# Kernel optimization log

Measured on AMD Instinct MI355X. Metric: run time of the kernel, lower is better.

Reference implementation:

```python
import jax, jax.numpy as jnp
import numpy as np

NX = 2048
NL = 20
BATCH = 512
EIGMAX = 10.0
EPS = 1e-9


def prox_cardan(eta, x):
    """Prox of u -> -eta*(log(u)+log(1-u)) at x: unique root in (0,1) of
    u^3 - (1+x)u^2 + (x-2eta)u + eta = 0 (Cardano / trigonometric method)."""
    b = -(1.0 + x)
    c = x - 2.0 * eta
    d = eta
    p = c - b * b / 3.0
    q = 2.0 * b ** 3 / 27.0 - b * c / 3.0 + d
    disc = -4.0 * p ** 3 - 27.0 * q ** 2
    # three-real-roots branch (trigonometric); requires p<0
    pm = jnp.minimum(p, -1e-12)
    m = 2.0 * jnp.sqrt(-pm / 3.0)
    arg = jnp.clip(3.0 * q / (pm * m), -1.0, 1.0)
    th = jnp.arccos(arg)
    k = jnp.arange(3, dtype=x.dtype)
    t_trig = m[..., None] * jnp.cos((th[..., None] - 2.0 * jnp.pi * k) / 3.0)
    r_trig = t_trig - b[..., None] / 3.0
    in01 = (r_trig > 0.0) & (r_trig < 1.0)
    idx = jnp.argmax(in01, axis=-1)
    root3 = jnp.take_along_axis(r_trig, idx[..., None], axis=-1)[..., 0]
    # one-real-root branch
    s = jnp.sqrt(jnp.maximum(q * q / 4.0 + p ** 3 / 27.0, 0.0))
    root1 = jnp.cbrt(-q / 2.0 + s) + jnp.cbrt(-q / 2.0 - s) - b / 3.0
    u = jnp.where(disc >= 0.0, root3, root1)
    return jnp.clip(u, EPS, 1.0 - EPS)


def setup_inputs() -> dict:
    key = jax.random.key(0)
    k1, k2, k3, k4, k5 = jax.random.split(key, 5)
    x = jax.random.uniform(k1, (BATCH, 1, NX), dtype=jnp.float32)
    # symmetric PSD operators for T^T T and D^T D (as in a discretized inverse problem)
    A = jax.random.normal(k2, (NX, NX), dtype=jnp.float32)
    tTT = (A @ A.T) / NX
    B = jax.random.normal(k3, (NX, NX), dtype=jnp.float32)
    tDD = (B @ B.T) / NX
    # orthogonal change-of-basis: element <-> eigen bases
    Q, _ = jnp.linalg.qr(jax.random.normal(k4, (NX, NX), dtype=jnp.float32))
    Pelt = Q.astype(jnp.float32)
    Peig = Q.T.astype(jnp.float32)
    x_b = jnp.einsum('ij,bcj->bci', tTT, x) + 0.01 * jax.random.normal(k5, (BATCH, 1, NX), dtype=jnp.float32)
    gamma = jnp.full((NL,), 0.1, dtype=jnp.float32)   # nn.Parameter([0.1])
    mu = jnp.zeros((NL,), dtype=jnp.float32)          # nn.Parameter([0.0])
    reg = jnp.full((NL,), 0.001, dtype=jnp.float32)   # noisy=True -> trainable 0.001
    return {"x": x, "x_b": x_b, "tDD": tDD, "tTT": tTT, "Peig": Peig,
            "Pelt": Pelt, "gamma": gamma, "mu": mu, "reg": reg}


def reference(x, x_b, tDD, tTT, Peig, Pelt, gamma, mu, reg):
    def step(xc, params):
        g_raw, mu_raw, reg_raw = params
        g = jax.nn.softplus(g_raw)
        mu_l = jax.nn.softplus(mu_raw) / 1e6
        reg_l = jax.nn.softplus(reg_raw) / (EIGMAX ** 2)
        grad = (jnp.einsum('ij,bcj->bci', tTT, xc) - x_b
                + reg_l * jnp.einsum('ij,bcj->bci', tDD, xc))
        xt = xc - g * grad
        xt = jnp.einsum('ij,bcj->bci', Pelt, xt)
        xt = prox_cardan(g * mu_l, xt)
        xt = jnp.einsum('ij,bcj->bci', Peig, xt)
        return xt, None

    out, _ = jax.lax.scan(step, x, (gamma, mu, reg))
    return out
```

## Files before the change

### kernel.cpp

```cpp
#include <hip/hip_runtime.h>
#include <math.h>

#define MDIM 512
#define NDIM 2048
#define KDIM 2048
#define NLAYERS 20

static const size_t MN = (size_t)MDIM * NDIM;
static const size_t OPN = (size_t)KDIM * KDIM;

using bf16x8 = __attribute__((ext_vector_type(8))) short;
using f32x4  = __attribute__((ext_vector_type(4))) float;

__device__ __forceinline__ double softplusd(double v) {
    return (v > 20.0) ? v : log1p(exp(v));
}

__device__ __forceinline__ float prox_cardan_f(float eta, float x) {
    const float b  = -(1.0f + x);
    const float c  = x - 2.0f * eta;
    const float dd = eta;
    const float p  = c - b * b * (1.0f / 3.0f);
    const float q  = 2.0f * b * b * b * (1.0f / 27.0f) - b * c * (1.0f / 3.0f) + dd;
    const float disc = -4.0f * p * p * p - 27.0f * q * q;
    const float pm = fminf(p, -1e-12f);
    const float mm = 2.0f * sqrtf(-pm * (1.0f / 3.0f));
    float arg = 3.0f * q / (pm * mm);
    arg = fminf(fmaxf(arg, -1.0f), 1.0f);
    const float th = acosf(arg);
    const float TWO_PI = 6.28318530717958647692f;
    const float r0 = mm * cosf(th * (1.0f / 3.0f)) - b * (1.0f / 3.0f);
    const float r1 = mm * cosf((th - TWO_PI) * (1.0f / 3.0f)) - b * (1.0f / 3.0f);
    const float r2 = mm * cosf((th - 2.0f * TWO_PI) * (1.0f / 3.0f)) - b * (1.0f / 3.0f);
    const bool in0 = (r0 > 0.0f) && (r0 < 1.0f);
    const bool in1 = (r1 > 0.0f) && (r1 < 1.0f);
    const bool in2 = (r2 > 0.0f) && (r2 < 1.0f);
    const float root3 = in0 ? r0 : (in1 ? r1 : (in2 ? r2 : r0));
    const float s = sqrtf(fmaxf(q * q * 0.25f + p * p * p * (1.0f / 27.0f), 0.0f));
    const float root1 = cbrtf(-q * 0.5f + s) + cbrtf(-q * 0.5f - s) - b * (1.0f / 3.0f);
    const float u = (disc >= 0.0f) ? root3 : root1;
    return fminf(fmaxf(u, 1e-9f), 1.0f - 1e-9f);
}

__device__ __forceinline__ double prox_newton_d(double eta, double x) {
    double u = (double)prox_cardan_f((float)eta, (float)x);
#pragma unroll
    for (int i = 0; i < 4; ++i) {
        const double um1 = u - 1.0;
        const double umx = u - x;
        const double P  = u * um1 * umx - eta * (2.0 * u - 1.0);
        const double dP = um1 * umx + u * umx + u * um1 - 2.0 * eta;
        u = u - P / dP;
        u = fmin(fmax(u, 1e-12), 1.0 - 1e-12);
    }
    return fmin(fmax(u, 1e-9), 1.0 - 1e-9);
}

__device__ __forceinline__ unsigned short f2bf(float f) {
    unsigned u = __float_as_uint(f);
    unsigned r = (u + 0x7FFFu + ((u >> 16) & 1u)) >> 16;
    return (unsigned short)r;
}
__device__ __forceinline__ float bf2f(unsigned short h) {
    return __uint_as_float(((unsigned)h) << 16);
}
__device__ __forceinline__ void split3f(float f, unsigned short& b1,
                                        unsigned short& b2, unsigned short& b3) {
    b1 = f2bf(f);
    const float r1 = f - bf2f(b1);
    b2 = f2bf(r1);
    const float r2 = r1 - bf2f(b2);
    b3 = f2bf(r2);
}

__device__ __forceinline__ void gl16(const void* g, void* l) {
    __builtin_amdgcn_global_load_lds(
        (const __attribute__((address_space(1))) unsigned int*)g,
        (__attribute__((address_space(3))) unsigned int*)l, 16, 0, 0);
}

__global__ __launch_bounds__(256) void split3_op(
    const float* __restrict__ s1, const float* __restrict__ s2,
    const float* __restrict__ greg, int layer,
    unsigned short* __restrict__ p1, unsigned short* __restrict__ p2,
    unsigned short* __restrict__ p3) {
    const size_t i = ((size_t)blockIdx.x * 256 + threadIdx.x) * 4;
    float reglf = 0.0f;
    if (s2) reglf = (float)(softplusd((double)greg[layer]) * 0.01);
    const float4 a = *(const float4*)(s1 + i);
    float4 b = make_float4(0.f, 0.f, 0.f, 0.f);
    if (s2) b = *(const float4*)(s2 + i);
    ushort4 o1, o2, o3;
    split3f(fmaf(reglf, b.x, a.x), o1.x, o2.x, o3.x);
    split3f(fmaf(reglf, b.y, a.y), o1.y, o2.y, o3.y);
    split3f(fmaf(reglf, b.z, a.z), o1.z, o2.z, o3.z);
    split3f(fmaf(reglf, b.w, a.w), o1.w, o2.w, o3.w);
    *(ushort4*)(p1 + i) = o1;
    *(ushort4*)(p2 + i) = o2;
    *(ushort4*)(p3 + i) = o3;
}

__global__ __launch_bounds__(256) void split3_w(
    const float* __restrict__ s1, const float* __restrict__ s2,
    const float* __restrict__ greg, int layer,
    unsigned short* __restrict__ p1, unsigned short* __restrict__ p2,
    unsigned short* __restrict__ p3) {
    if (layer > 0 && greg[layer] == greg[0]) return;
    const size_t i = ((size_t)blockIdx.x * 256 + threadIdx.x) * 4;
    const float reglf = (float)(softplusd((double)greg[layer]) * 0.01);
    const float4 a = *(const float4*)(s1 + i);
    const float4 b = *(const float4*)(s2 + i);
    ushort4 o1, o2, o3;
    split3f(fmaf(reglf, b.x, a.x), o1.x, o2.x, o3.x);
    split3f(fmaf(reglf, b.y, a.y), o1.y, o2.y, o3.y);
    split3f(fmaf(reglf, b.z, a.z), o1.z, o2.z, o3.z);
    split3f(fmaf(reglf, b.w, a.w), o1.w, o2.w, o3.w);
    *(ushort4*)(p1 + i) = o1;
    *(ushort4*)(p2 + i) = o2;
    *(ushort4*)(p3 + i) = o3;
}

__global__ __launch_bounds__(256, 3) void gemm_bf16x3(
    const unsigned short* __restrict__ A1, const unsigned short* __restrict__ A2,
    const unsigned short* __restrict__ A3,
    const unsigned short* __restrict__ W1, const unsigned short* __restrict__ W2,
    const unsigned short* __restrict__ W3,
    float* __restrict__ Part, int klen, int S) {
    __shared__ __align__(16) unsigned short Ab[2][3][64][32];
    __shared__ __align__(16) unsigned short Wb[2][3][64][32];

    const int tid = threadIdx.x;

    const int nwg = 256 * S;
    const int cpx = nwg >> 3;
    const int bid = blockIdx.x;
    const int g   = (bid & 7) * cpx + (bid >> 3);
    const int xs  = g / (8 * S);
    const int rr  = g - xs * (8 * S);
    const int ys  = rr & 7;
    const int zs  = rr >> 3;
    const int n0 = xs * 64;
    const int m0 = ys * 64;
    const int kb = zs * klen;

    const int lane = tid & 63, wid = tid >> 6;
    const int quad = lane >> 4, lrow = lane & 15;
    const int wm = (wid >> 1) * 32, wn = (wid & 1) * 32;

    const int srow = tid >> 2;
    const int lc8  = ((tid & 3) ^ ((tid >> 3) & 3)) * 8;
    const int t8   = tid * 8;
    const int qx   = (quad ^ ((lrow >> 1) & 3)) * 8;

    const unsigned short* gA1 = A1 + (size_t)(m0 + srow) * KDIM + kb + lc8;
    const unsigned short* gA2 = A2 + (size_t)(m0 + srow) * KDIM + kb + lc8;
    const unsigned short* gA3 = A3 + (size_t)(m0 + srow) * KDIM + kb + lc8;
    const unsigned short* gW1 = W1 + (size_t)(n0 + srow) * KDIM + kb + lc8;
    const unsigned short* gW2 = W2 + (size_t)(n0 + srow) * KDIM + kb + lc8;
    const unsigned short* gW3 = W3 + (size_t)(n0 + srow) * KDIM + kb + lc8;

    unsigned short* lA = &Ab[0][0][0][0];
    unsigned short* lW = &Wb[0][0][0][0];

    f32x4 ahi[2][2], alo[2][2];
#pragma unroll
    for (int a = 0; a < 2; ++a)
#pragma unroll
        for (int b = 0; b < 2; ++b) {
            ahi[a][b] = (f32x4){0.f, 0.f, 0.f, 0.f};
            alo[a][b] = (f32x4){0.f, 0.f, 0.f, 0.f};
        }

    gl16(gA1, lA + t8);
    gl16(gA2, lA + 2048 + t8);
    gl16(gA3, lA + 4096 + t8);
    gl16(gW1, lW + t8);
    gl16(gW2, lW + 2048 + t8);
    gl16(gW3, lW + 4096 + t8);

    int cur = 0;
    for (int k0 = 0; k0 < klen; k0 += 32) {
        __syncthreads();

        if (k0 + 32 < klen) {
            const int nb = (cur ^ 1) * 6144;
            gl16(gA1 + k0 + 32, lA + nb + t8);
            gl16(gA2 + k0 + 32, lA + nb + 2048 + t8);
            gl16(gA3 + k0 + 32, lA + nb + 4096 + t8);
            gl16(gW1 + k0 + 32, lW + nb + t8);
            gl16(gW2 + k0 + 32, lW + nb + 2048 + t8);
            gl16(gW3 + k0 + 32, lW + nb + 4096 + t8);
        }

        const unsigned short* cA = lA + cur * 6144;
        const unsigned short* cW = lW + cur * 6144;

        bf16x8 fa[2][3], fw[2][3];
#pragma unroll
        for (int t = 0; t < 2; ++t) {
            const int ra = (wm + t * 16 + lrow) * 32;
            const int rw = (wn + t * 16 + lrow) * 32;
            fa[t][0] = *(const bf16x8*)(cA + ra + qx);
            fa[t][1] = *(const bf16x8*)(cA + 2048 + ra + qx);
            fa[t][2] = *(const bf16x8*)(cA + 4096 + ra + qx);
            fw[t][0] = *(const bf16x8*)(cW + rw + qx);
            fw[t][1] = *(const bf16x8*)(cW + 2048 + rw + qx);
            fw[t][2] = *(const bf16x8*)(cW + 4096 + rw + qx);
        }
#pragma unroll
        for (int tm = 0; tm < 2; ++tm)
#pragma unroll
            for (int tn = 0; tn < 2; ++tn) {
                ahi[tm][tn] = __builtin_amdgcn_mfma_f32_16x16x32_bf16(fa[tm][0], fw[tn][0], ahi[tm][tn], 0, 0, 0);
                alo[tm][tn] = __builtin_amdgcn_mfma_f32_16x16x32_bf16(fa[tm][0], fw[tn][1], alo[tm][tn], 0, 0, 0);
                alo[tm][tn] = __builtin_amdgcn_mfma_f32_16x16x32_bf16(fa[tm][1], fw[tn][0], alo[tm][tn], 0, 0, 0);
                alo[tm][tn] = __builtin_amdgcn_mfma_f32_16x16x32_bf16(fa[tm][1], fw[tn][1], alo[tm][tn], 0, 0, 0);
                alo[tm][tn] = __builtin_amdgcn_mfma_f32_16x16x32_bf16(fa[tm][0], fw[tn][2], alo[tm][tn], 0, 0, 0);
                alo[tm][tn] = __builtin_amdgcn_mfma_f32_16x16x32_bf16(fa[tm][2], fw[tn][0], alo[tm][tn], 0, 0, 0);
            }
        cur ^= 1;
    }

    float* P = Part + (size_t)zs * MN;
#pragma unroll
    for (int tm = 0; tm < 2; ++tm)
#pragma unroll
        for (int tn = 0; tn < 2; ++tn) {
            const int mbase = m0 + wm + tm * 16 + quad * 4;
            const int nn = n0 + wn + tn * 16 + lrow;
#pragma unroll
            for (int r = 0; r < 4; ++r)
                P[(size_t)(mbase + r) * NDIM + nn] = ahi[tm][tn][r] + alo[tm][tn][r];
        }
}

template <int MODE>
__global__ __launch_bounds__(256) void combine3(
    const float* __restrict__ Part, int S,
    const float* __restrict__ Xc, const float* __restrict__ Xb,
    float* __restrict__ stateOut,
    unsigned short* __restrict__ p1, unsigned short* __restrict__ p2,
    unsigned short* __restrict__ p3,
    const float* __restrict__ gam, const float* __restrict__ gmu,
    const float* __restrict__ greg, int layer) {
    const size_t i = ((size_t)blockIdx.x * 256 + threadIdx.x) * 4;
    double s0 = 0.0, s1 = 0.0, s2 = 0.0, s3 = 0.0;
    for (int z = 0; z < S; ++z) {
        const float4 p = *(const float4*)(Part + (size_t)z * MN + i);
        s0 += (double)p.x; s1 += (double)p.y; s2 += (double)p.z; s3 += (double)p.w;
    }
    float v0, v1, v2, v3;
    if (MODE == 0) {
        const double g = softplusd((double)gam[layer]);
        const float4 xc = *(const float4*)(Xc + i);
        const float4 xb = *(const float4*)(Xb + i);
        v0 = (float)((double)xc.x - g * (s0 - (double)xb.x));
        v1 = (float)((double)xc.y - g * (s1 - (double)xb.y));
        v2 = (float)((double)xc.z - g * (s2 - (double)xb.z));
        v3 = (float)((double)xc.w - g * (s3 - (double)xb.w));
    } else if (MODE == 1) {
        const double g   = softplusd((double)gam[layer]);
        const double eta = g * softplusd((double)gmu[layer]) * 1e-6;
        v0 = (float)prox_newton_d(eta, s0);
        v1 = (float)prox_newton_d(eta, s1);
        v2 = (float)prox_newton_d(eta, s2);
        v3 = (float)prox_newton_d(eta, s3);
    } else {
        v0 = (float)s0; v1 = (float)s1; v2 = (float)s2; v3 = (float)s3;
        *(float4*)(stateOut + i) = make_float4(v0, v1, v2, v3);
    }
    ushort4 o1, o2, o3;
    split3f(v0, o1.x, o2.x, o3.x);
    split3f(v1, o1.y, o2.y, o3.y);
    split3f(v2, o1.z, o2.z, o3.z);
    split3f(v3, o1.w, o2.w, o3.w);
    *(ushort4*)(p1 + i) = o1;
    *(ushort4*)(p2 + i) = o2;
    *(ushort4*)(p3 + i) = o3;
}

#define BM 64
#define BN 64
#define BK 32
#define LDSP 68

__device__ __forceinline__ double prox_cardan_d(double eta, double x) {
    const double b  = -(1.0 + x);
    const double c  = x - 2.0 * eta;
    const double dd = eta;
    const double p  = c - b * b * (1.0 / 3.0);
    const double q  = 2.0 * b * b * b * (1.0 / 27.0) - b * c * (1.0 / 3.0) + dd;
    const double disc = -4.0 * p * p * p - 27.0 * q * q;
    const double pm = fmin(p, -1e-12);
    const double mm = 2.0 * sqrt(-pm * (1.0 / 3.0));
    double arg = 3.0 * q / (pm * mm);
    arg = fmin(fmax(arg, -1.0), 1.0);
    const double th = acos(arg);
    const double TWO_PI = 6.283185307179586476925286766559;
    const double r0 = mm * cos(th * (1.0 / 3.0)) - b * (1.0 / 3.0);
    const double r1 = mm * cos((th - TWO_PI) * (1.0 / 3.0)) - b * (1.0 / 3.0);
    const double r2 = mm * cos((th - 2.0 * TWO_PI) * (1.0 / 3.0)) - b * (1.0 / 3.0);
    const bool in0 = (r0 > 0.0) && (r0 < 1.0);
    const bool in1 = (r1 > 0.0) && (r1 < 1.0);
    const bool in2 = (r2 > 0.0) && (r2 < 1.0);
    const double root3 = in0 ? r0 : (in1 ? r1 : (in2 ? r2 : r0));
    const double s = sqrt(fmax(q * q * 0.25 + p * p * p * (1.0 / 27.0), 0.0));
    const double root1 = cbrt(-q * 0.5 + s) + cbrt(-q * 0.5 - s) - b * (1.0 / 3.0);
    const double u = (disc >= 0.0) ? root3 : root1;
    return fmin(fmax(u, 1e-9), 1.0 - 1e-9);
}

template <bool FUSE2>
__global__ __launch_bounds__(256, 4) void gemm_nt_splitk(
    const float* __restrict__ A, const float* __restrict__ W1,
    const float* __restrict__ W2, double* __restrict__ Part,
    const float* __restrict__ greg, int layer, int klen) {
    __shared__ float As[BK][LDSP];
    __shared__ float Ws[BK][LDSP];
    const int tid = threadIdx.x;
    const int m0 = blockIdx.y * BM;
    const int n0 = blockIdx.x * BN;
    const int kbase = blockIdx.z * klen;
    float reglf = 0.0f;
    if (FUSE2) reglf = (float)(softplusd((double)greg[layer]) * 0.01);
    const int lrow = tid >> 3;
    const int lkc  = (tid & 7) << 2;
    const float* pA  = A  + (size_t)(m0 + lrow) * KDIM + kbase + lkc;
    const float* pW  = W1 + (size_t)(n0 + lrow) * KDIM + kbase + lkc;
    const float* pW2 = FUSE2 ? (W2 + (size_t)(n0 + lrow) * KDIM + kbase + lkc) : nullptr;
    float4 ra[2], rw[2];
    ra[0] = *(const float4*)(pA);
    ra[1] = *(const float4*)(pA + 32 * KDIM);
    rw[0] = *(const float4*)(pW);
    rw[1] = *(const float4*)(pW + 32 * KDIM);
    if (FUSE2) {
        const float4 u0 = *(const float4*)(pW2);
        const float4 u1 = *(const float4*)(pW2 + 32 * KDIM);
        rw[0].x += reglf * u0.x; rw[0].y += reglf * u0.y;
        rw[0].z += reglf * u0.z; rw[0].w += reglf * u0.w;
        rw[1].x += reglf * u1.x; rw[1].y += reglf * u1.y;
        rw[1].z += reglf * u1.z; rw[1].w += reglf * u1.w;
    }
    float  acc[4][4]   = {};
    double acc64[4][4] = {};
    const int tx = (tid & 15) << 2;
    const int ty = (tid >> 4) << 2;
    int it = 0;
    for (int k0 = 0; k0 < klen; k0 += BK, ++it) {
#pragma unroll
        for (int h = 0; h < 2; ++h) {
            const int row = lrow + (h << 5);
            As[lkc + 0][row] = (h ? ra[1].x : ra[0].x);
            As[lkc + 1][row] = (h ? ra[1].y : ra[0].y);
            As[lkc + 2][row] = (h ? ra[1].z : ra[0].z);
            As[lkc + 3][row] = (h ? ra[1].w : ra[0].w);
            Ws[lkc + 0][row] = (h ? rw[1].x : rw[0].x);
            Ws[lkc + 1][row] = (h ? rw[1].y : rw[0].y);
            Ws[lkc + 2][row] = (h ? rw[1].z : rw[0].z);
            Ws[lkc + 3][row] = (h ? rw[1].w : rw[0].w);
        }
        __syncthreads();
        if (k0 + BK < klen) {
            const float* qA = pA + k0 + BK;
            ra[0] = *(const float4*)(qA);
            ra[1] = *(const float4*)(qA + 32 * KDIM);
            const float* qW = pW + k0 + BK;
            rw[0] = *(const float4*)(qW);
            rw[1] = *(const float4*)(qW + 32 * KDIM);
            if (FUSE2) {
                const float* qW2 = pW2 + k0 + BK;
                const float4 u0 = *(const float4*)(qW2);
                const float4 u1 = *(const float4*)(qW2 + 32 * KDIM);
                rw[0].x += reglf * u0.x; rw[0].y += reglf * u0.y;
                rw[0].z += reglf * u0.z; rw[0].w += reglf * u0.w;
                rw[1].x += reglf * u1.x; rw[1].y += reglf * u1.y;
                rw[1].z += reglf * u1.z; rw[1].w += reglf * u1.w;
            }
        }
#pragma unroll
        for (int kk = 0; kk < BK; ++kk) {
            const float4 a4 = *(const float4*)(&As[kk][ty]);
            const float4 b4 = *(const float4*)(&Ws[kk][tx]);
            const float av[4] = {a4.x, a4.y, a4.z, a4.w};
            const float bv[4] = {b4.x, b4.y, b4.z, b4.w};
#pragma unroll
            for (int r = 0; r < 4; ++r)
#pragma unroll
                for (int cc = 0; cc < 4; ++cc)
                    acc[r][cc] = fmaf(av[r], bv[cc], acc[r][cc]);
        }
        __syncthreads();
        if ((it & 1) == 1) {
#pragma unroll
            for (int r = 0; r < 4; ++r)
#pragma unroll
                for (int cc = 0; cc < 4; ++cc) {
                    acc64[r][cc] += (double)acc[r][cc];
                    acc[r][cc] = 0.0f;
                }
        }
    }
#pragma unroll
    for (int r = 0; r < 4; ++r)
#pragma unroll
        for (int cc = 0; cc < 4; ++cc)
            acc64[r][cc] += (double)acc[r][cc];
    double* Pz = Part + (size_t)blockIdx.z * MN;
#pragma unroll
    for (int r = 0; r < 4; ++r) {
        double* q = Pz + (size_t)(m0 + ty + r) * NDIM + n0 + tx;
        *(double2*)(q)     = make_double2(acc64[r][0], acc64[r][1]);
        *(double2*)(q + 2) = make_double2(acc64[r][2], acc64[r][3]);
    }
}

template <int MODE>
__global__ __launch_bounds__(256) void combine_ep(
    const double* __restrict__ Part, int nslices,
    const float* __restrict__ Xc, const float* __restrict__ Xb,
    float* __restrict__ Out,
    const float* __restrict__ gam, const float* __restrict__ gmu,
    const float* __restrict__ greg, int layer) {
    const size_t i4 = ((size_t)blockIdx.x * 256 + threadIdx.x) * 4;
    double s0 = 0.0, s1 = 0.0, s2 = 0.0, s3 = 0.0;
    for (int z = 0; z < nslices; ++z) {
        const double* p = Part + (size_t)z * MN + i4;
        const double2 a = *(const double2*)(p);
        const double2 b = *(const double2*)(p + 2);
        s0 += a.x; s1 += a.y; s2 += b.x; s3 += b.y;
    }
    float4 o;
    if (MODE == 0) {
        const double g = softplusd((double)gam[layer]);
        const float4 xc = *(const float4*)(Xc + i4);
        const float4 xb = *(const float4*)(Xb + i4);
        o.x = (float)((double)xc.x - g * (s0 - (double)xb.x));
        o.y = (float)((double)xc.y - g * (s1 - (double)xb.y));
        o.z = (float)((double)xc.z - g * (s2 - (double)xb.z));
        o.w = (float)((double)xc.w - g * (s3 - (double)xb.w));
    } else if (MODE == 1) {
        const double g   = softplusd((double)gam[layer]);
        const double eta = g * softplusd((double)gmu[layer]) * 1e-6;
        o.x = (float)prox_cardan_d(eta, s0);
        o.y = (float)prox_cardan_d(eta, s1);
        o.z = (float)prox_cardan_d(eta, s2);
        o.w = (float)prox_cardan_d(eta, s3);
    } else {
        o.x = (float)s0; o.y = (float)s1; o.z = (float)s2; o.w = (float)s3;
    }
    *(float4*)(Out + i4) = o;
}

extern "C" void kernel_launch(void* const* d_in, const int* in_sizes, int n_in,
                              void* d_out, int out_size, void* d_ws, size_t ws_size,
                              hipStream_t stream) {
    const float* x    = (const float*)d_in[0];
    const float* x_b  = (const float*)d_in[1];
    const float* tDD  = (const float*)d_in[2];
    const float* tTT  = (const float*)d_in[3];
    const float* Peig = (const float*)d_in[4];
    const float* Pelt = (const float*)d_in[5];
    const float* gam  = (const float*)d_in[6];
    const float* gmu  = (const float*)d_in[7];
    const float* greg = (const float*)d_in[8];
    float* out = (float*)d_out;

    const size_t TRI_OP_B = 3 * OPN * 2;
    const size_t TRI_A_B  = 3 * MN * 2;
    const size_t STATE_B  = MN * 4;
    const size_t full_need = 3 * TRI_OP_B + 2 * TRI_A_B + STATE_B + 2 * MN * 4;
    const size_t mid_need  = 1 * TRI_OP_B + 2 * TRI_A_B + STATE_B + 2 * MN * 4;

    const bool full = (ws_size >= full_need);
    const bool mid  = (!full && ws_size >= mid_need);

    if (full || mid) {
        const int S = 2;
        const int klen = KDIM / S;
        char* p = (char*)d_ws;
        unsigned short *Wt1, *Wt2, *Wt3, *Pe1, *Pe2, *Pe3, *Pg1, *Pg2, *Pg3;
        if (full) {
            Wt1 = (unsigned short*)p;        Wt2 = Wt1 + OPN; Wt3 = Wt2 + OPN; p += TRI_OP_B;
            Pe1 = (unsigned short*)p;        Pe2 = Pe1 + OPN; Pe3 = Pe2 + OPN; p += TRI_OP_B;
            Pg1 = (unsigned short*)p;        Pg2 = Pg1 + OPN; Pg3 = Pg2 + OPN; p += TRI_OP_B;
        } else {
            Wt1 = (unsigned short*)p;        Wt2 = Wt1 + OPN; Wt3 = Wt2 + OPN; p += TRI_OP_B;
            Pe1 = Wt1; Pe2 = Wt2; Pe3 = Wt3;
            Pg1 = Wt1; Pg2 = Wt2; Pg3 = Wt3;
        }
        unsigned short* Aa1 = (unsigned short*)p; unsigned short* Aa2 = Aa1 + MN;
        unsigned short* Aa3 = Aa2 + MN; p += TRI_A_B;
        unsigned short* Ab1 = (unsigned short*)p; unsigned short* Ab2 = Ab1 + MN;
        unsigned short* Ab3 = Ab2 + MN; p += TRI_A_B;
        float* state = (float*)p; p += STATE_B;
        float* part  = (float*)p;

        const dim3 gg((unsigned)(256 * S));
        const unsigned cgrid = (unsigned)(MN / 4 / 256);
        const unsigned ogrid = (unsigned)(OPN / 4 / 256);

        split3_op<<<cgrid, 256, 0, stream>>>(x, nullptr, greg, 0, Aa1, Aa2, Aa3);
        if (full) {
            split3_op<<<ogrid, 256, 0, stream>>>(Pelt, nullptr, greg, 0, Pe1, Pe2, Pe3);
            split3_op<<<ogrid, 256, 0, stream>>>(Peig, nullptr, greg, 0, Pg1, Pg2, Pg3);
        }

        unsigned short *c1 = Aa1, *c2 = Aa2, *c3 = Aa3;
        unsigned short *d1 = Ab1, *d2 = Ab2, *d3 = Ab3;

        for (int l = 0; l < NLAYERS; ++l) {
            if (full) {
                split3_w<<<ogrid, 256, 0, stream>>>(tTT, tDD, greg, l, Wt1, Wt2, Wt3);
            } else {
                split3_op<<<ogrid, 256, 0, stream>>>(tTT, tDD, greg, l, Wt1, Wt2, Wt3);
            }
            gemm_bf16x3<<<gg, 256, 0, stream>>>(c1, c2, c3, Wt1, Wt2, Wt3, part, klen, S);
            combine3<0><<<cgrid, 256, 0, stream>>>(part, S, (l == 0 ? x : state), x_b,
                                                   nullptr, d1, d2, d3, gam, gmu, greg, l);
            if (mid) split3_op<<<ogrid, 256, 0, stream>>>(Pelt, nullptr, greg, 0, Pe1, Pe2, Pe3);
            gemm_bf16x3<<<gg, 256, 0, stream>>>(d1, d2, d3, Pe1, Pe2, Pe3, part, klen, S);
            combine3<1><<<cgrid, 256, 0, stream>>>(part, S, nullptr, nullptr,
                                                   nullptr, c1, c2, c3, gam, gmu, greg, l);
            if (mid) split3_op<<<ogrid, 256, 0, stream>>>(Peig, nullptr, greg, 0, Pg1, Pg2, Pg3);
            gemm_bf16x3<<<gg, 256, 0, stream>>>(c1, c2, c3, Pg1, Pg2, Pg3, part, klen, S);
            combine3<2><<<cgrid, 256, 0, stream>>>(part, S, nullptr, nullptr,
                                                   (l == NLAYERS - 1 ? out : state),
                                                   d1, d2, d3, gam, gmu, greg, l);
            unsigned short* t;
            t = c1; c1 = d1; d1 = t;
            t = c2; c2 = d2; d2 = t;
            t = c3; c3 = d3; d3 = t;
        }
        return;
    }

    char* wsb = (char*)d_ws;
    float* b0 = (float*)wsb;
    float* b1 = b0 + MN;
    float* b2 = b1 + MN;
    float* b3 = b2 + MN;
    const size_t base_bytes = 4 * MN * sizeof(float);
    double* partd = (double*)(wsb + base_bytes);
    int S = 0;
    if (ws_size >= base_bytes + 2 * MN * sizeof(double)) S = 2;
    else if (ws_size >= base_bytes + 1 * MN * sizeof(double)) S = 1;
    if (S == 0) return;
    const int klen = KDIM / S;
    dim3 gg(NDIM / BN, MDIM / BM, S);
    dim3 cg((unsigned)(MN / 4 / 256));
    const float* cur = x;
    float* bx = b0; float* bu = b1; float* bn = b2; float* bo = b3;
    for (int l = 0; l < NLAYERS; ++l) {
        gemm_nt_splitk<true><<<gg, 256, 0, stream>>>(cur, tTT, tDD, partd, greg, l, klen);
        combine_ep<0><<<cg, 256, 0, stream>>>(partd, S, cur, x_b, bx, gam, gmu, greg, l);
        gemm_nt_splitk<false><<<gg, 256, 0, stream>>>(bx, Pelt, nullptr, partd, greg, l, klen);
        combine_ep<1><<<cg, 256, 0, stream>>>(partd, S, nullptr, nullptr, bu, gam, gmu, greg, l);
        gemm_nt_splitk<false><<<gg, 256, 0, stream>>>(bu, Peig, nullptr, partd, greg, l, klen);
        float* dst = (l == NLAYERS - 1) ? out : bn;
        combine_ep<2><<<cg, 256, 0, stream>>>(partd, S, nullptr, nullptr, dst, gam, gmu, greg, l);
        cur = bn;
        float* t = bn; bn = bo; bo = t;
    }
}
```

Measured before the change: 2.620 ms.

## Triple-buffer LDS in bf16x3 GEMM with explicit vmcnt waits and MFMA priority

Replaces the double-buffered K loop of the split-bf16 GEMM with a three-stage LDS ring, prefetching two steps ahead and using explicit s_waitcnt vmcnt counts plus a raw barrier instead of __syncthreads. MFMA sections are wrapped in s_setprio to favour compute issue. The extra stage raises LDS use per block, so launch bounds drop from 3 to 2 blocks per CU, trading occupancy for deeper latency hiding. The hand-written vmcnt(6) assumes exactly six outstanding loads per stage, which is fragile if gl16 lowers to a different number of memory ops.

```diff
diff --git a/kernel.cpp b/kernel.cpp
--- a/kernel.cpp
+++ b/kernel.cpp
@@ -120,14 +120,14 @@
     *(ushort4*)(p3 + i) = o3;
 }
 
-__global__ __launch_bounds__(256, 3) void gemm_bf16x3(
+__global__ __launch_bounds__(256, 2) void gemm_bf16x3(
     const unsigned short* __restrict__ A1, const unsigned short* __restrict__ A2,
     const unsigned short* __restrict__ A3,
     const unsigned short* __restrict__ W1, const unsigned short* __restrict__ W2,
     const unsigned short* __restrict__ W3,
     float* __restrict__ Part, int klen, int S) {
-    __shared__ __align__(16) unsigned short Ab[2][3][64][32];
-    __shared__ __align__(16) unsigned short Wb[2][3][64][32];
+    __shared__ __align__(16) unsigned short Ab[3][3][64][32];
+    __shared__ __align__(16) unsigned short Wb[3][3][64][32];
 
     const int tid = threadIdx.x;
 
@@ -171,29 +171,39 @@
             alo[a][b] = (f32x4){0.f, 0.f, 0.f, 0.f};
         }
 
-    gl16(gA1, lA + t8);
-    gl16(gA2, lA + 2048 + t8);
-    gl16(gA3, lA + 4096 + t8);
-    gl16(gW1, lW + t8);
-    gl16(gW2, lW + 2048 + t8);
-    gl16(gW3, lW + 4096 + t8);
-
-    int cur = 0;
-    for (int k0 = 0; k0 < klen; k0 += 32) {
-        __syncthreads();
-
-        if (k0 + 32 < klen) {
-            const int nb = (cur ^ 1) * 6144;
-            gl16(gA1 + k0 + 32, lA + nb + t8);
-            gl16(gA2 + k0 + 32, lA + nb + 2048 + t8);
-            gl16(gA3 + k0 + 32, lA + nb + 4096 + t8);
-            gl16(gW1 + k0 + 32, lW + nb + t8);
-            gl16(gW2 + k0 + 32, lW + nb + 2048 + t8);
-            gl16(gW3 + k0 + 32, lW + nb + 4096 + t8);
-        }
-
-        const unsigned short* cA = lA + cur * 6144;
-        const unsigned short* cW = lW + cur * 6144;
+    auto stage = [&](int buf, int step) {
+        const int off = buf * 6144;
+        const int ko  = step * 32;
+        gl16(gA1 + ko, lA + off + t8);
+        gl16(gA2 + ko, lA + off + 2048 + t8);
+        gl16(gA3 + ko, lA + off + 4096 + t8);
+        gl16(gW1 + ko, lW + off + t8);
+        gl16(gW2 + ko, lW + off + 2048 + t8);
+        gl16(gW3 + ko, lW + off + 4096 + t8);
+    };
+
+    const int nsteps = klen >> 5;
+
+    stage(0, 0);
+    if (nsteps > 1) stage(1, 1);
+
+    int idx = 0;
+    for (int s = 0; s < nsteps; ++s) {
+        if (s + 1 < nsteps) {
+            asm volatile("s_waitcnt vmcnt(6)" ::: "memory");
+        } else {
+            asm volatile("s_waitcnt vmcnt(0)" ::: "memory");
+        }
+        __builtin_amdgcn_s_barrier();
+        __builtin_amdgcn_sched_barrier(0);
+
+        if (s + 2 < nsteps) {
+            int pre = idx + 2; if (pre >= 3) pre -= 3;
+            stage(pre, s + 2);
+        }
+
+        const unsigned short* cA = lA + idx * 6144;
+        const unsigned short* cW = lW + idx * 6144;
 
         bf16x8 fa[2][3], fw[2][3];
 #pragma unroll
@@ -207,6 +217,7 @@
             fw[t][1] = *(const bf16x8*)(cW + 2048 + rw + qx);
             fw[t][2] = *(const bf16x8*)(cW + 4096 + rw + qx);
         }
+        __builtin_amdgcn_s_setprio(1);
 #pragma unroll
         for (int tm = 0; tm < 2; ++tm)
 #pragma unroll
@@ -218,7 +229,9 @@
                 alo[tm][tn] = __builtin_amdgcn_mfma_f32_16x16x32_bf16(fa[tm][0], fw[tn][2], alo[tm][tn], 0, 0, 0);
                 alo[tm][tn] = __builtin_amdgcn_mfma_f32_16x16x32_bf16(fa[tm][2], fw[tn][0], alo[tm][tn], 0, 0, 0);
             }
-        cur ^= 1;
+        __builtin_amdgcn_s_setprio(0);
+
+        ++idx; if (idx == 3) idx = 0;
     }
 
     float* P = Part + (size_t)zs * MN;
```

Result: slower. 2.719 ms (+3.8%).

## Replace async LDS DMA double-buffer with register-staged prefetch and 64-wide K tiles

Applied to the files above, without the earlier changes.

The GEMM main loop no longer uses global_load_lds double buffering with 32-wide K slices. It now prefetches the next 64-wide K tile into registers while computing on a single XOR-swizzled LDS buffer, and raises MFMA priority with s_setprio. Occupancy hint drops from 3 to 2 blocks per CU. The goal is fewer barriers per K step and better overlap of global loads with MFMA, at the cost of more registers and a serial store-then-compute phase per tile.

```diff
diff --git a/kernel.cpp b/kernel.cpp
--- a/kernel.cpp
+++ b/kernel.cpp
@@ -73,12 +73,6 @@
     b3 = f2bf(r2);
 }
 
-__device__ __forceinline__ void gl16(const void* g, void* l) {
-    __builtin_amdgcn_global_load_lds(
-        (const __attribute__((address_space(1))) unsigned int*)g,
-        (__attribute__((address_space(3))) unsigned int*)l, 16, 0, 0);
-}
-
 __global__ __launch_bounds__(256) void split3_op(
     const float* __restrict__ s1, const float* __restrict__ s2,
     const float* __restrict__ greg, int layer,
@@ -120,14 +114,14 @@
     *(ushort4*)(p3 + i) = o3;
 }
 
-__global__ __launch_bounds__(256, 3) void gemm_bf16x3(
+__global__ __launch_bounds__(256, 2) void gemm_bf16x3(
     const unsigned short* __restrict__ A1, const unsigned short* __restrict__ A2,
     const unsigned short* __restrict__ A3,
     const unsigned short* __restrict__ W1, const unsigned short* __restrict__ W2,
     const unsigned short* __restrict__ W3,
     float* __restrict__ Part, int klen, int S) {
-    __shared__ __align__(16) unsigned short Ab[2][3][64][32];
-    __shared__ __align__(16) unsigned short Wb[2][3][64][32];
+    __shared__ __align__(16) unsigned short Ab[3][64][64];
+    __shared__ __align__(16) unsigned short Wb[3][64][64];
 
     const int tid = threadIdx.x;
 
@@ -148,77 +142,95 @@
     const int wm = (wid >> 1) * 32, wn = (wid & 1) * 32;
 
     const int srow = tid >> 2;
-    const int lc8  = ((tid & 3) ^ ((tid >> 3) & 3)) * 8;
-    const int t8   = tid * 8;
-    const int qx   = (quad ^ ((lrow >> 1) & 3)) * 8;
-
-    const unsigned short* gA1 = A1 + (size_t)(m0 + srow) * KDIM + kb + lc8;
-    const unsigned short* gA2 = A2 + (size_t)(m0 + srow) * KDIM + kb + lc8;
-    const unsigned short* gA3 = A3 + (size_t)(m0 + srow) * KDIM + kb + lc8;
-    const unsigned short* gW1 = W1 + (size_t)(n0 + srow) * KDIM + kb + lc8;
-    const unsigned short* gW2 = W2 + (size_t)(n0 + srow) * KDIM + kb + lc8;
-    const unsigned short* gW3 = W3 + (size_t)(n0 + srow) * KDIM + kb + lc8;
-
-    unsigned short* lA = &Ab[0][0][0][0];
-    unsigned short* lW = &Wb[0][0][0][0];
+    const int sc   = tid & 3;
+    const int sswz = srow & 7;
+    const int rswz = lrow & 7;
+
+    const unsigned short* gA1 = A1 + (size_t)(m0 + srow) * KDIM + kb + sc * 8;
+    const unsigned short* gA2 = A2 + (size_t)(m0 + srow) * KDIM + kb + sc * 8;
+    const unsigned short* gA3 = A3 + (size_t)(m0 + srow) * KDIM + kb + sc * 8;
+    const unsigned short* gW1 = W1 + (size_t)(n0 + srow) * KDIM + kb + sc * 8;
+    const unsigned short* gW2 = W2 + (size_t)(n0 + srow) * KDIM + kb + sc * 8;
+    const unsigned short* gW3 = W3 + (size_t)(n0 + srow) * KDIM + kb + sc * 8;
 
     f32x4 ahi[2][2], alo[2][2];
 #pragma unroll
     for (int a = 0; a < 2; ++a)
 #pragma unroll
-        for (int b = 0; b < 2; ++b) {
-            ahi[a][b] = (f32x4){0.f, 0.f, 0.f, 0.f};
-            alo[a][b] = (f32x4){0.f, 0.f, 0.f, 0.f};
-        }
-
-    gl16(gA1, lA + t8);
-    gl16(gA2, lA + 2048 + t8);
-    gl16(gA3, lA + 4096 + t8);
-    gl16(gW1, lW + t8);
-    gl16(gW2, lW + 2048 + t8);
-    gl16(gW3, lW + 4096 + t8);
-
-    int cur = 0;
-    for (int k0 = 0; k0 < klen; k0 += 32) {
+        for (int b2 = 0; b2 < 2; ++b2) {
+            ahi[a][b2] = (f32x4){0.f, 0.f, 0.f, 0.f};
+            alo[a][b2] = (f32x4){0.f, 0.f, 0.f, 0.f};
+        }
+
+    bf16x8 ra[3][2], rw[3][2];
+#pragma unroll
+    for (int h = 0; h < 2; ++h) {
+        ra[0][h] = *(const bf16x8*)(gA1 + h * 32);
+        ra[1][h] = *(const bf16x8*)(gA2 + h * 32);
+        ra[2][h] = *(const bf16x8*)(gA3 + h * 32);
+        rw[0][h] = *(const bf16x8*)(gW1 + h * 32);
+        rw[1][h] = *(const bf16x8*)(gW2 + h * 32);
+        rw[2][h] = *(const bf16x8*)(gW3 + h * 32);
+    }
+
+    const int nref = klen >> 6;
+
+    for (int r = 0; r < nref; ++r) {
         __syncthreads();
-
-        if (k0 + 32 < klen) {
-            const int nb = (cur ^ 1) * 6144;
-            gl16(gA1 + k0 + 32, lA + nb + t8);
-            gl16(gA2 + k0 + 32, lA + nb + 2048 + t8);
-            gl16(gA3 + k0 + 32, lA + nb + 4096 + t8);
-            gl16(gW1 + k0 + 32, lW + nb + t8);
-            gl16(gW2 + k0 + 32, lW + nb + 2048 + t8);
-            gl16(gW3 + k0 + 32, lW + nb + 4096 + t8);
-        }
-
-        const unsigned short* cA = lA + cur * 6144;
-        const unsigned short* cW = lW + cur * 6144;
-
-        bf16x8 fa[2][3], fw[2][3];
-#pragma unroll
-        for (int t = 0; t < 2; ++t) {
-            const int ra = (wm + t * 16 + lrow) * 32;
-            const int rw = (wn + t * 16 + lrow) * 32;
-            fa[t][0] = *(const bf16x8*)(cA + ra + qx);
-            fa[t][1] = *(const bf16x8*)(cA + 2048 + ra + qx);
-            fa[t][2] = *(const bf16x8*)(cA + 4096 + ra + qx);
-            fw[t][0] = *(const bf16x8*)(cW + rw + qx);
-            fw[t][1] = *(const bf16x8*)(cW + 2048 + rw + qx);
-            fw[t][2] = *(const bf16x8*)(cW + 4096 + rw + qx);
-        }
-#pragma unroll
-        for (int tm = 0; tm < 2; ++tm)
-#pragma unroll
-            for (int tn = 0; tn < 2; ++tn) {
-                ahi[tm][tn] = __builtin_amdgcn_mfma_f32_16x16x32_bf16(fa[tm][0], fw[tn][0], ahi[tm][tn], 0, 0, 0);
-                alo[tm][tn] = __builtin_amdgcn_mfma_f32_16x16x32_bf16(fa[tm][0], fw[tn][1], alo[tm][tn], 0, 0, 0);
-                alo[tm][tn] = __builtin_amdgcn_mfma_f32_16x16x32_bf16(fa[tm][1], fw[tn][0], alo[tm][tn], 0, 0, 0);
-                alo[tm][tn] = __builtin_amdgcn_mfma_f32_16x16x32_bf16(fa[tm][1], fw[tn][1], alo[tm][tn], 0, 0, 0);
-                alo[tm][tn] = __builtin_amdgcn_mfma_f32_16x16x32_bf16(fa[tm][0], fw[tn][2], alo[tm][tn], 0, 0, 0);
-                alo[tm][tn] = __builtin_amdgcn_mfma_f32_16x16x32_bf16(fa[tm][2], fw[tn][0], alo[tm][tn], 0, 0, 0);
+#pragma unroll
+        for (int h = 0; h < 2; ++h) {
+            const int gp = (((sc + 4 * h) ^ sswz) * 8);
+            *(bf16x8*)&Ab[0][srow][gp] = ra[0][h];
+            *(bf16x8*)&Ab[1][srow][gp] = ra[1][h];
+            *(bf16x8*)&Ab[2][srow][gp] = ra[2][h];
+            *(bf16x8*)&Wb[0][srow][gp] = rw[0][h];
+            *(bf16x8*)&Wb[1][srow][gp] = rw[1][h];
+            *(bf16x8*)&Wb[2][srow][gp] = rw[2][h];
+        }
+        __syncthreads();
+
+        if (r + 1 < nref) {
+            const int ko = (r + 1) * 64;
+#pragma unroll
+            for (int h = 0; h < 2; ++h) {
+                ra[0][h] = *(const bf16x8*)(gA1 + ko + h * 32);
+                ra[1][h] = *(const bf16x8*)(gA2 + ko + h * 32);
+                ra[2][h] = *(const bf16x8*)(gA3 + ko + h * 32);
+                rw[0][h] = *(const bf16x8*)(gW1 + ko + h * 32);
+                rw[1][h] = *(const bf16x8*)(gW2 + ko + h * 32);
+                rw[2][h] = *(const bf16x8*)(gW3 + ko + h * 32);
             }
-        cur ^= 1;
+        }
+
+#pragma unroll
+        for (int kk = 0; kk < 2; ++kk) {
+            bf16x8 fa[2][3], fw[2][3];
+#pragma unroll
+            for (int t = 0; t < 2; ++t) {
+                const int raw = wm + t * 16 + lrow;
+                const int rww = wn + t * 16 + lrow;
+                const int gp = (((kk * 4 + quad) ^ rswz) * 8);
+                fa[t][0] = *(const bf16x8*)&Ab[0][raw][gp];
+                fa[t][1] = *(const bf16x8*)&Ab[1][raw][gp];
+                fa[t][2] = *(const bf16x8*)&Ab[2][raw][gp];
+                fw[t][0] = *(const bf16x8*)&Wb[0][rww][gp];
+                fw[t][1] = *(const bf16x8*)&Wb[1][rww][gp];
+                fw[t][2] = *(const bf16x8*)&Wb[2][rww][gp];
+            }
+            __builtin_amdgcn_s_setprio(1);
+#pragma unroll
+            for (int tm = 0; tm < 2; ++tm)
+#pragma unroll
+                for (int tn = 0; tn < 2; ++tn) {
+                    ahi[tm][tn] = __builtin_amdgcn_mfma_f32_16x16x32_bf16(fa[tm][0], fw[tn][0], ahi[tm][tn], 0, 0, 0);
+                    alo[tm][tn] = __builtin_amdgcn_mfma_f32_16x16x32_bf16(fa[tm][0], fw[tn][1], alo[tm][tn], 0, 0, 0);
+                    alo[tm][tn] = __builtin_amdgcn_mfma_f32_16x16x32_bf16(fa[tm][1], fw[tn][0], alo[tm][tn], 0, 0, 0);
+                    alo[tm][tn] = __builtin_amdgcn_mfma_f32_16x16x32_bf16(fa[tm][1], fw[tn][1], alo[tm][tn], 0, 0, 0);
+                    alo[tm][tn] = __builtin_amdgcn_mfma_f32_16x16x32_bf16(fa[tm][0], fw[tn][2], alo[tm][tn], 0, 0, 0);
+                    alo[tm][tn] = __builtin_amdgcn_mfma_f32_16x16x32_bf16(fa[tm][2], fw[tn][0], alo[tm][tn], 0, 0, 0);
+                }
+            __builtin_amdgcn_s_setprio(0);
+        }
     }
 
     float* P = Part + (size_t)zs * MN;
@@ -229,8 +241,8 @@
             const int mbase = m0 + wm + tm * 16 + quad * 4;
             const int nn = n0 + wn + tn * 16 + lrow;
 #pragma unroll
-            for (int r = 0; r < 4; ++r)
-                P[(size_t)(mbase + r) * NDIM + nn] = ahi[tm][tn][r] + alo[tm][tn][r];
+            for (int r2 = 0; r2 < 4; ++r2)
+                P[(size_t)(mbase + r2) * NDIM + nn] = ahi[tm][tn][r2] + alo[tm][tn][r2];
         }
 }
 
```

Result: faster. 2.493 ms (-4.8%).
